# Kernel tuning notes

Hardware: AMD Instinct MI355X
Metric: run time of the kernel (lower is better)

The kernel has to match this reference:

```python
import jax, jax.numpy as jnp
import numpy as np
from jax import lax

B, N, CIN, H, W = 1, 6, 256, 32, 88
COUT = 80
IMG_H, IMG_W = 256, 704
XB = (-51.2, 51.2, 0.8); YB = (-51.2, 51.2, 0.8); ZB = (-5.0, 3.0, 0.8)
NX, NY, NZ = 128, 128, 10
EPS = 1e-5


def _voxel_coords(b0, b1, vs):
    n = int(round((b1 - b0) / vs))
    return jnp.linspace(b0 + 0.5 * vs, b1 - 0.5 * vs, n, dtype=jnp.float32)


def _make_points():
    xs = _voxel_coords(*XB); ys = _voxel_coords(*YB); zs = _voxel_coords(*ZB)
    gx, gy, gz = jnp.meshgrid(xs, ys, zs, indexing='ij')
    return jnp.stack([gx, gy, gz], -1).reshape(-1, 3)  # [M,3], M = NX*NY*NZ


def _conv(x, w, b=None, pad=1):
    y = lax.conv_general_dilated(x, w, (1, 1), [(pad, pad), (pad, pad)],
                                 dimension_numbers=('NCHW', 'OIHW', 'NCHW'))
    if b is not None:
        y = y + b[None, :, None, None]
    return y


def _bn(x, g, b, m, v):
    return (g[None, :, None, None] * (x - m[None, :, None, None])
            * lax.rsqrt(v[None, :, None, None] + EPS) + b[None, :, None, None])


def _bilinear(feat, gx, gy):
    # feat [C,Hf,Wf]; gx,gy [M] in [-1,1]; align_corners=True, zero padding
    C, Hf, Wf = feat.shape
    ix = (gx + 1.0) * 0.5 * (Wf - 1)
    iy = (gy + 1.0) * 0.5 * (Hf - 1)
    ix0 = jnp.floor(ix); iy0 = jnp.floor(iy)
    wx1 = ix - ix0; wy1 = iy - iy0

    def tap(iyf, ixf, wgt):
        valid = (ixf >= 0) & (ixf < Wf) & (iyf >= 0) & (iyf < Hf)
        ii = jnp.clip(ixf, 0, Wf - 1).astype(jnp.int32)
        jj = jnp.clip(iyf, 0, Hf - 1).astype(jnp.int32)
        return feat[:, jj, ii] * (wgt * valid)[None, :]

    return (tap(iy0, ix0, (1 - wy1) * (1 - wx1))
            + tap(iy0, ix0 + 1, (1 - wy1) * wx1)
            + tap(iy0 + 1, ix0, wy1 * (1 - wx1))
            + tap(iy0 + 1, ix0 + 1, wy1 * wx1))


def reference(img, lidar2image, w1, b1, g1, beta1, m1, v1,
              w2, b2, g2, beta2, m2, v2, w3, b3):
    # proj_net: conv3x3+BN+ReLU, conv3x3+BN+ReLU, conv1x1
    x = img.reshape(B * N, CIN, H, W)
    x = jax.nn.relu(_bn(_conv(x, w1, b1), g1, beta1, m1, v1))
    x = jax.nn.relu(_bn(_conv(x, w2, b2), g2, beta2, m2, v2))
    feat = _conv(x, w3, b3, pad=0)  # [B*N, COUT, H, W]

    pts = _make_points()  # [M,3]
    R = lidar2image[:, :, :3, :3].reshape(B * N, 3, 3)
    t = lidar2image[:, :, :3, 3].reshape(B * N, 3, 1)
    proj = jnp.einsum('kij,mj->kim', R, pts) + t  # [BN,3,M]
    dist = proj[:, 2]
    px = proj[:, 0] / dist
    py = proj[:, 1] / dist
    gx = px / IMG_W * 2.0 - 1.0
    gy = py / IMG_H * 2.0 - 1.0

    sampled = jax.vmap(_bilinear)(feat, gx, gy)  # [BN, COUT, M]
    on_img = (px < IMG_W) & (px > 0) & (py < IMG_H) & (py > 0) & (dist > 0.1)
    sampled = jnp.where(on_img[:, None, :], sampled, 0.0)

    vox = sampled.reshape(B, N, COUT, NX, NY, NZ)
    bev = jnp.max(vox, axis=1).mean(axis=-1)  # [B, COUT, NX, NY]
    return bev


def setup_inputs() -> dict:
    key = jax.random.key(0)
    ks = jax.random.split(key, 8)
    img = jax.random.normal(ks[0], (B, N, CIN, H, W), jnp.float32)

    # Plausible lidar->image matrices: 6 cameras in a ring, pinhole intrinsics.
    fx = fy = 280.0; cx = IMG_W / 2.0; cy = IMG_H / 2.0
    K = np.array([[fx, 0.0, cx], [0.0, fy, cy], [0.0, 0.0, 1.0]])
    mats = []
    for k in range(N):
        th = 2.0 * np.pi * k / N
        fwd = np.array([np.cos(th), np.sin(th), 0.0])
        rgt = np.array([np.sin(th), -np.cos(th), 0.0])
        dwn = np.array([0.0, 0.0, -1.0])
        Rm = np.stack([rgt, dwn, fwd], 0)
        c = np.array([0.5 * np.cos(th), 0.5 * np.sin(th), 1.5])
        M4 = np.eye(4)
        M4[:3, :3] = K @ Rm
        M4[:3, 3] = K @ (-Rm @ c)
        mats.append(M4)
    lidar2image = jnp.asarray(np.broadcast_to(np.stack(mats), (B, N, 4, 4)).copy(),
                              jnp.float32)

    def w(k, shape, s=0.02):
        return jax.random.normal(k, shape, jnp.float32) * s

    zc = lambda c: jnp.zeros((c,), jnp.float32)
    oc = lambda c: jnp.ones((c,), jnp.float32)
    return dict(
        img=img, lidar2image=lidar2image,
        w1=w(ks[1], (CIN, CIN, 3, 3)), b1=zc(CIN),
        g1=oc(CIN), beta1=zc(CIN), m1=zc(CIN), v1=oc(CIN),
        w2=w(ks[2], (CIN, CIN, 3, 3)), b2=zc(CIN),
        g2=oc(CIN), beta2=zc(CIN), m2=zc(CIN), v2=oc(CIN),
        w3=w(ks[3], (COUT, CIN, 1, 1)), b3=zc(COUT),
    )
```

## Files before the change

### kernel.cpp

```cpp
#include <hip/hip_runtime.h>
#include <math.h>

#define N_IMG 6
#define CIN   256
#define H_IN  32
#define W_IN  88
#define SP    2816
#define HH    34
#define WW    90
#define SPH   3060
#define COUTC 80
#define EPSBN 1e-5f

typedef _Float16 half8 __attribute__((ext_vector_type(8)));
typedef float floatx4 __attribute__((ext_vector_type(4)));

#define AS1 __attribute__((address_space(1)))
#define AS3 __attribute__((address_space(3)))

__global__ __launch_bounds__(256) void prep_w33(const float* __restrict__ wa,
                                                const float* __restrict__ wb,
                                                _Float16* __restrict__ wTa,
                                                _Float16* __restrict__ wTb) {
  __shared__ float s[2304];
  const int oc = blockIdx.x;
  const int tid = threadIdx.x;
  const float* w = blockIdx.y ? wb : wa;
  _Float16* wT = blockIdx.y ? wTb : wTa;
  const float* wo = w + (size_t)oc * 2304;
  for (int i = tid; i < 2304; i += 256) s[i] = wo[i];
  __syncthreads();
  for (int i = tid; i < 2304; i += 256) {
    const int tap = i >> 8;
    const int ic  = i & 255;
    wT[((size_t)tap * 256 + oc) * 256 + ic] = (_Float16)s[ic * 9 + tap];
  }
}

__global__ __launch_bounds__(256) void prep_misc(const float* __restrict__ w3,
                                                 _Float16* __restrict__ wT3,
                                                 _Float16* __restrict__ a,
                                                 _Float16* __restrict__ b) {
  const int bx = blockIdx.x;
  const int tid = threadIdx.x;
  if (bx < 80) {
    const int idx = bx * 256 + tid;
    wT3[idx] = (_Float16)w3[idx];
  } else {
    const int im = bx - 80;
    for (int s = tid; s < 244 * 32; s += 256) {
      const int pos = s >> 5;
      const int gr  = s & 31;
      int h, w;
      if (pos < 90)       { h = 0;  w = pos; }
      else if (pos < 180) { h = 33; w = pos - 90; }
      else { const int r = pos - 180; h = 1 + (r >> 1); w = (r & 1) * 89; }
      const size_t off = ((size_t)im * SPH + h * WW + w) * CIN + gr * 8;
      half8 z = {};
      *(half8*)(a + off) = z;
      *(half8*)(b + off) = z;
    }
  }
}

__global__ __launch_bounds__(256) void nchw_to_nhwc(const float* __restrict__ img,
                                                    _Float16* __restrict__ x0) {
  __shared__ float t[64][65];
  const int sp0 = blockIdx.x * 64;
  const int ic0 = blockIdx.y * 64;
  const int im  = blockIdx.z;
  const int tx = threadIdx.x & 63;
  const int ty = threadIdx.x >> 6;
  for (int r = ty; r < 64; r += 4)
    t[r][tx] = img[((size_t)(im * CIN + ic0 + r)) * SP + sp0 + tx];
  __syncthreads();
  for (int r = ty; r < 64; r += 4) {
    const int sp = sp0 + r;
    const int h = sp / 88;
    const int w = sp - h * 88;
    x0[((size_t)im * SPH + h * WW + w + WW + 1) * CIN + ic0 + tx] = (_Float16)t[tx][r];
  }
}

__global__ __launch_bounds__(256) void conv3x3_mfma(
    const _Float16* __restrict__ x, const _Float16* __restrict__ wT,
    const float* __restrict__ bias, const float* __restrict__ gamma,
    const float* __restrict__ beta, const float* __restrict__ bnm,
    const float* __restrict__ bnv, _Float16* __restrict__ out,
    int OW, int OB, int imStride)
{
  __shared__ _Float16 As[2][64 * 64];
  __shared__ _Float16 Bs[2][128 * 64];

  const int tid  = threadIdx.x;
  const int wv   = tid >> 6;
  const int lane = tid & 63;
  const int bx   = blockIdx.x;
  const int n0   = (bx & 1) << 7;
  const int mt   = bx >> 1;
  const int im   = mt / 44;
  const int m0sp = (mt - im * 44) * 64;
  const _Float16* xim = x + (size_t)im * SPH * CIN;

  int srcA[2], srcB[4];
  #pragma unroll
  for (int i = 0; i < 2; ++i) {
    const int g = i * 256 + wv * 64 + lane;
    const int row = g >> 3;
    const int lg  = (g & 7) ^ (row & 7);
    const int m = m0sp + row;
    const int h = m / 88;
    const int w = m - h * 88;
    srcA[i] = ((h + 1) * WW + (w + 1)) * CIN + lg * 8;
  }
  #pragma unroll
  for (int i = 0; i < 4; ++i) {
    const int g = i * 256 + wv * 64 + lane;
    const int row = g >> 3;
    const int lg  = (g & 7) ^ (row & 7);
    srcB[i] = (n0 + row) * 256 + lg * 8;
  }

  const int fr = lane & 15;
  const int q  = lane >> 4;
  const int q4 = q * 4;
  const int mw = (wv & 1) * 32;
  const int nw = (wv >> 1) * 64;

  floatx4 acc[2][4];
  #pragma unroll
  for (int i = 0; i < 2; ++i)
    #pragma unroll
    for (int j = 0; j < 4; ++j) {
      acc[i][j][0] = 0.f; acc[i][j][1] = 0.f; acc[i][j][2] = 0.f; acc[i][j][3] = 0.f;
    }

  {
    const int aoff0 = (-1 * WW - 1) * CIN;
    #pragma unroll
    for (int i = 0; i < 2; ++i)
      __builtin_amdgcn_global_load_lds(
          (const AS1 void*)(xim + srcA[i] + aoff0),
          (AS3 void*)(&As[0][(i * 256 + wv * 64) * 8]), 16, 0, 0);
    #pragma unroll
    for (int i = 0; i < 4; ++i)
      __builtin_amdgcn_global_load_lds(
          (const AS1 void*)(wT + srcB[i]),
          (AS3 void*)(&Bs[0][(i * 256 + wv * 64) * 8]), 16, 0, 0);
  }

  for (int c = 0; c < 36; ++c) {
    __syncthreads();
    if (c < 35) {
      const int cn   = c + 1;
      const int tapn = cn >> 2;
      const int iccn = (cn & 3) << 6;
      const int dyn  = tapn / 3 - 1;
      const int dxn  = tapn - (tapn / 3) * 3 - 1;
      const int aoffn = (dyn * WW + dxn) * CIN + iccn;
      const size_t boffn = (size_t)tapn * 65536 + iccn;
      const int nb = cn & 1;
      #pragma unroll
      for (int i = 0; i < 2; ++i)
        __builtin_amdgcn_global_load_lds(
            (const AS1 void*)(xim + srcA[i] + aoffn),
            (AS3 void*)(&As[nb][(i * 256 + wv * 64) * 8]), 16, 0, 0);
      #pragma unroll
      for (int i = 0; i < 4; ++i)
        __builtin_amdgcn_global_load_lds(
            (const AS1 void*)(wT + boffn + srcB[i]),
            (AS3 void*)(&Bs[nb][(i * 256 + wv * 64) * 8]), 16, 0, 0);
    }
    const int cb = c & 1;
    #pragma unroll
    for (int ks = 0; ks < 2; ++ks) {
      half8 af[2], bf[4];
      #pragma unroll
      for (int i = 0; i < 2; ++i) {
        const int row = mw + i * 16 + fr;
        af[i] = *(const half8*)(&As[cb][row * 64 + (((ks * 4 + q) ^ (row & 7)) * 8)]);
      }
      #pragma unroll
      for (int j = 0; j < 4; ++j) {
        const int row = nw + j * 16 + fr;
        bf[j] = *(const half8*)(&Bs[cb][row * 64 + (((ks * 4 + q) ^ (row & 7)) * 8)]);
      }
      #pragma unroll
      for (int i = 0; i < 2; ++i)
        #pragma unroll
        for (int j = 0; j < 4; ++j)
          acc[i][j] = __builtin_amdgcn_mfma_f32_16x16x32_f16(af[i], bf[j], acc[i][j], 0, 0, 0);
    }
  }

  #pragma unroll
  for (int j = 0; j < 4; ++j) {
    const int oc = n0 + nw + j * 16 + fr;
    const float sc = gamma[oc] * rsqrtf(bnv[oc] + EPSBN);
    const float sh = (bias[oc] - bnm[oc]) * sc + beta[oc];
    #pragma unroll
    for (int i = 0; i < 2; ++i) {
      #pragma unroll
      for (int r = 0; r < 4; ++r) {
        const int m = m0sp + mw + i * 16 + q4 + r;
        const int h = m / 88;
        const int w = m - h * 88;
        const float v = fmaxf(fmaf(acc[i][j][r], sc, sh), 0.f);
        out[((size_t)im * imStride + h * OW + w + OB) * CIN + oc] = (_Float16)v;
      }
    }
  }
}

__global__ __launch_bounds__(128) void conv1x1_mfma(
    const _Float16* __restrict__ x, const _Float16* __restrict__ wT,
    const float* __restrict__ bias, _Float16* __restrict__ feat)
{
  __shared__ _Float16 Bs[80 * 264];

  const int tid = threadIdx.x;
  const int m0  = blockIdx.x * 64;
  const int wv   = tid >> 6;
  const int lane = tid & 63;
  const int fr  = lane & 15;
  const int q8  = (lane >> 4) * 8;
  const int q4  = (lane >> 4) * 4;

  for (int g = tid; g < 2560; g += 128) {
    const int oc = g >> 5;
    const int kg8 = (g & 31) << 3;
    *(half8*)(&Bs[oc * 264 + kg8]) = *(const half8*)(wT + oc * 256 + kg8);
  }
  __syncthreads();

  floatx4 acc[2][5];
  #pragma unroll
  for (int i = 0; i < 2; ++i)
    #pragma unroll
    for (int j = 0; j < 5; ++j) {
      acc[i][j][0] = 0.f; acc[i][j][1] = 0.f; acc[i][j][2] = 0.f; acc[i][j][3] = 0.f;
    }

  const _Float16* xa = x + (size_t)(m0 + wv * 32 + fr) * 256 + q8;
  #pragma unroll
  for (int ks = 0; ks < 8; ++ks) {
    half8 af[2], bf[5];
    #pragma unroll
    for (int i = 0; i < 2; ++i)
      af[i] = *(const half8*)(xa + (size_t)i * 16 * 256 + ks * 32);
    #pragma unroll
    for (int j = 0; j < 5; ++j)
      bf[j] = *(const half8*)(&Bs[(j * 16 + fr) * 264 + ks * 32 + q8]);
    #pragma unroll
    for (int i = 0; i < 2; ++i)
      #pragma unroll
      for (int j = 0; j < 5; ++j)
        acc[i][j] = __builtin_amdgcn_mfma_f32_16x16x32_f16(af[i], bf[j], acc[i][j], 0, 0, 0);
  }

  #pragma unroll
  for (int j = 0; j < 5; ++j) {
    const int oc = j * 16 + fr;
    const float bb = bias[oc];
    #pragma unroll
    for (int i = 0; i < 2; ++i) {
      const int mbase = m0 + wv * 32 + i * 16 + q4;
      #pragma unroll
      for (int r = 0; r < 4; ++r)
        feat[(size_t)(mbase + r) * COUTC + oc] = (_Float16)(acc[i][j][r] + bb);
    }
  }
}

__global__ __launch_bounds__(320) void bev_sample(
    const _Float16* __restrict__ feat, const float* __restrict__ l2i,
    float* __restrict__ tmp)
{
  __shared__ int4   eo[1920];
  __shared__ float4 ew[1920];
  const int tid = threadIdx.x;
  const int cellBase = blockIdx.x * 32;

  for (int e = tid; e < 1920; e += 320) {
    const int cell = e / 60;
    const int idx = e - cell * 60;
    const int n = idx / 10;
    const int z = idx - n * 10;
    const int cid = cellBase + cell;
    const int gix = cid >> 7;
    const int giy = cid & 127;
    const float X = (float)(-50.8 + (double)gix * (101.6 / 127.0));
    const float Y = (float)(-50.8 + (double)giy * (101.6 / 127.0));
    const float Z = (float)(-4.6 + (double)z * (7.2 / 9.0));
    const float* M = l2i + n * 16;
    const float pw = M[0] * X + M[1] * Y + M[2] * Z + M[3];
    const float ph = M[4] * X + M[5] * Y + M[6] * Z + M[7];
    const float d  = M[8] * X + M[9] * Y + M[10] * Z + M[11];
    const float px = pw / d;
    const float py = ph / d;
    const bool on_img = (px < 704.f) && (px > 0.f) && (py < 256.f) && (py > 0.f) && (d > 0.1f);
    const float gx = px / 704.f * 2.f - 1.f;
    const float gy = py / 256.f * 2.f - 1.f;
    const float ixf = (gx + 1.f) * 0.5f * 87.f;
    const float iyf = (gy + 1.f) * 0.5f * 31.f;
    const float ix0 = floorf(ixf);
    const float iy0 = floorf(iyf);
    const float wx1 = ixf - ix0;
    const float wy1 = iyf - iy0;
    const float ix1 = ix0 + 1.f, iy1 = iy0 + 1.f;
    float w00 = (1.f - wy1) * (1.f - wx1);
    float w01 = (1.f - wy1) * wx1;
    float w10 = wy1 * (1.f - wx1);
    float w11 = wy1 * wx1;
    const bool vx0 = (ix0 >= 0.f) && (ix0 < 88.f);
    const bool vx1 = (ix1 >= 0.f) && (ix1 < 88.f);
    const bool vy0 = (iy0 >= 0.f) && (iy0 < 32.f);
    const bool vy1 = (iy1 >= 0.f) && (iy1 < 32.f);
    if (!(on_img && vy0 && vx0)) w00 = 0.f;
    if (!(on_img && vy0 && vx1)) w01 = 0.f;
    if (!(on_img && vy1 && vx0)) w10 = 0.f;
    if (!(on_img && vy1 && vx1)) w11 = 0.f;
    const int i0 = (int)fminf(fmaxf(ix0, 0.f), 87.f);
    const int i1 = (int)fminf(fmaxf(ix1, 0.f), 87.f);
    const int j0 = (int)fminf(fmaxf(iy0, 0.f), 31.f);
    const int j1 = (int)fminf(fmaxf(iy1, 0.f), 31.f);
    const int base = n * SP;
    eo[e] = make_int4((base + j0 * 88 + i0) * COUTC,
                      (base + j0 * 88 + i1) * COUTC,
                      (base + j1 * 88 + i0) * COUTC,
                      (base + j1 * 88 + i1) * COUTC);
    ew[e] = make_float4(w00, w01, w10, w11);
  }
  __syncthreads();

  const int grp  = tid % 10;
  const int c8   = grp * 8;
  const int cell = tid / 10;
  const int ebase = cell * 60;
  float acc[8];
  #pragma unroll
  for (int k = 0; k < 8; ++k) acc[k] = 0.f;

  for (int z = 0; z < 10; ++z) {
    float mx[8];
    #pragma unroll
    for (int k = 0; k < 8; ++k) mx[k] = -INFINITY;
    #pragma unroll
    for (int n = 0; n < 6; ++n) {
      const float4 w = ew[ebase + n * 10 + z];
      if (w.x + w.y + w.z + w.w > 0.f) {
        const int4 o = eo[ebase + n * 10 + z];
        const half8 p00 = *(const half8*)(feat + o.x + c8);
        const half8 p01 = *(const half8*)(feat + o.y + c8);
        const half8 p10 = *(const half8*)(feat + o.z + c8);
        const half8 p11 = *(const half8*)(feat + o.w + c8);
        #pragma unroll
        for (int k = 0; k < 8; ++k) {
          float v = w.x * (float)p00[k];
          v = fmaf(w.y, (float)p01[k], v);
          v = fmaf(w.z, (float)p10[k], v);
          v = fmaf(w.w, (float)p11[k], v);
          mx[k] = fmaxf(mx[k], v);
        }
      } else {
        #pragma unroll
        for (int k = 0; k < 8; ++k) mx[k] = fmaxf(mx[k], 0.f);
      }
    }
    #pragma unroll
    for (int k = 0; k < 8; ++k) acc[k] += mx[k];
  }
  const int cid = cellBase + cell;
  float* op = tmp + (size_t)cid * COUTC + c8;
  #pragma unroll
  for (int k = 0; k < 8; ++k) op[k] = acc[k] * 0.1f;
}

__global__ __launch_bounds__(256) void bev_transpose(const float* __restrict__ tmp,
                                                     float* __restrict__ out)
{
  __shared__ float tile[32][33];
  const int mBase = blockIdx.x * 32;
  const int cBase = blockIdx.y * 32;
  const int tx = threadIdx.x & 31;
  const int ty = threadIdx.x >> 5;
  for (int i = ty; i < 32; i += 8) {
    const int cc = cBase + tx;
    tile[i][tx] = (cc < COUTC) ? tmp[(size_t)(mBase + i) * COUTC + cc] : 0.f;
  }
  __syncthreads();
  for (int i = ty; i < 32; i += 8) {
    const int cc = cBase + i;
    if (cc < COUTC) out[(size_t)cc * 16384 + mBase + tx] = tile[tx][i];
  }
}

extern "C" void kernel_launch(void* const* d_in, const int* in_sizes, int n_in,
                              void* d_out, int out_size, void* d_ws, size_t ws_size,
                              hipStream_t stream)
{
  const float* img = (const float*)d_in[0];
  const float* l2i = (const float*)d_in[1];
  const float* w1  = (const float*)d_in[2];
  const float* b1  = (const float*)d_in[3];
  const float* g1  = (const float*)d_in[4];
  const float* be1 = (const float*)d_in[5];
  const float* m1  = (const float*)d_in[6];
  const float* v1  = (const float*)d_in[7];
  const float* w2  = (const float*)d_in[8];
  const float* b2  = (const float*)d_in[9];
  const float* g2  = (const float*)d_in[10];
  const float* be2 = (const float*)d_in[11];
  const float* m2  = (const float*)d_in[12];
  const float* v2  = (const float*)d_in[13];
  const float* w3  = (const float*)d_in[14];
  const float* b3  = (const float*)d_in[15];

  char* ws = (char*)d_ws;
  _Float16* wT1h = (_Float16*)ws;  ws += (size_t)9 * CIN * CIN * 2;
  _Float16* wT2h = (_Float16*)ws;  ws += (size_t)9 * CIN * CIN * 2;
  _Float16* wT3h = (_Float16*)ws;  ws += (size_t)CIN * COUTC * 2;
  _Float16* x0   = (_Float16*)ws;  ws += (size_t)N_IMG * SPH * CIN * 2;
  _Float16* x1h  = (_Float16*)ws;  ws += (size_t)N_IMG * SPH * CIN * 2;
  _Float16* x2h  = (_Float16*)ws;  ws += (size_t)N_IMG * SP * CIN * 2;
  _Float16* feat = (_Float16*)ws;  ws += (size_t)N_IMG * SP * COUTC * 2;
  float*    tmp  = (float*)ws;
  float*    outp = (float*)d_out;

  prep_misc<<<86, 256, 0, stream>>>(w3, wT3h, x0, x1h);
  prep_w33<<<dim3(256, 2), 256, 0, stream>>>(w1, w2, wT1h, wT2h);
  nchw_to_nhwc<<<dim3(44, 4, 6), 256, 0, stream>>>(img, x0);

  conv3x3_mfma<<<528, 256, 0, stream>>>(x0, wT1h, b1, g1, be1, m1, v1,
                                        x1h, WW, WW + 1, SPH);
  conv3x3_mfma<<<528, 256, 0, stream>>>(x1h, wT2h, b2, g2, be2, m2, v2,
                                        x2h, 88, 0, SP);
  conv1x1_mfma<<<264, 128, 0, stream>>>(x2h, wT3h, b3, feat);

  bev_sample<<<512, 320, 0, stream>>>(feat, l2i, tmp);
  bev_transpose<<<dim3(512, 3), 256, 0, stream>>>(tmp, outp);
}
```

Measured before the change: 221.9 us.

## Split conv3x3 reduction over K into three partials with separate BN reduce

Each 3x3 conv's 36-step K loop is split across three blocks (blockIdx.y), raising the grid from 528 to 1584 blocks so more of the 256 CUs stay busy. Each split writes fp16 partial sums to a workspace buffer, and a new reduce_bn kernel adds the three partials, applies bias, BN and ReLU, and writes the padded NHWC output. The cost is extra global traffic for the partials (about 26 MB written and read per conv), two extra launches, and some precision loss from rounding partials to fp16.

```diff
diff --git a/kernel.cpp b/kernel.cpp
--- a/kernel.cpp
+++ b/kernel.cpp
@@ -82,12 +82,9 @@
   }
 }
 
-__global__ __launch_bounds__(256) void conv3x3_mfma(
+__global__ __launch_bounds__(256) void conv3x3_split(
     const _Float16* __restrict__ x, const _Float16* __restrict__ wT,
-    const float* __restrict__ bias, const float* __restrict__ gamma,
-    const float* __restrict__ beta, const float* __restrict__ bnm,
-    const float* __restrict__ bnv, _Float16* __restrict__ out,
-    int OW, int OB, int imStride)
+    _Float16* __restrict__ part)
 {
   __shared__ _Float16 As[2][64 * 64];
   __shared__ _Float16 Bs[2][128 * 64];
@@ -96,6 +93,7 @@
   const int wv   = tid >> 6;
   const int lane = tid & 63;
   const int bx   = blockIdx.x;
+  const int s    = blockIdx.y;
   const int n0   = (bx & 1) << 7;
   const int mt   = bx >> 1;
   const int im   = mt / 44;
@@ -135,8 +133,15 @@
       acc[i][j][0] = 0.f; acc[i][j][1] = 0.f; acc[i][j][2] = 0.f; acc[i][j][3] = 0.f;
     }
 
+  const int c0 = s * 12;
+
   {
-    const int aoff0 = (-1 * WW - 1) * CIN;
+    const int tap0 = c0 >> 2;
+    const int icc0 = (c0 & 3) << 6;
+    const int dy0  = tap0 / 3 - 1;
+    const int dx0  = tap0 - (tap0 / 3) * 3 - 1;
+    const int aoff0 = (dy0 * WW + dx0) * CIN + icc0;
+    const size_t boff0 = (size_t)tap0 * 65536 + icc0;
     #pragma unroll
     for (int i = 0; i < 2; ++i)
       __builtin_amdgcn_global_load_lds(
@@ -145,21 +150,21 @@
     #pragma unroll
     for (int i = 0; i < 4; ++i)
       __builtin_amdgcn_global_load_lds(
-          (const AS1 void*)(wT + srcB[i]),
+          (const AS1 void*)(wT + boff0 + srcB[i]),
           (AS3 void*)(&Bs[0][(i * 256 + wv * 64) * 8]), 16, 0, 0);
   }
 
-  for (int c = 0; c < 36; ++c) {
+  for (int lc = 0; lc < 12; ++lc) {
     __syncthreads();
-    if (c < 35) {
-      const int cn   = c + 1;
+    if (lc < 11) {
+      const int cn   = c0 + lc + 1;
       const int tapn = cn >> 2;
       const int iccn = (cn & 3) << 6;
       const int dyn  = tapn / 3 - 1;
       const int dxn  = tapn - (tapn / 3) * 3 - 1;
       const int aoffn = (dyn * WW + dxn) * CIN + iccn;
       const size_t boffn = (size_t)tapn * 65536 + iccn;
-      const int nb = cn & 1;
+      const int nb = (lc + 1) & 1;
       #pragma unroll
       for (int i = 0; i < 2; ++i)
         __builtin_amdgcn_global_load_lds(
@@ -171,7 +176,7 @@
             (const AS1 void*)(wT + boffn + srcB[i]),
             (AS3 void*)(&Bs[nb][(i * 256 + wv * 64) * 8]), 16, 0, 0);
     }
-    const int cb = c & 1;
+    const int cb = lc & 1;
     #pragma unroll
     for (int ks = 0; ks < 2; ++ks) {
       half8 af[2], bf[4];
@@ -193,23 +198,57 @@
     }
   }
 
+  _Float16* pb = part + ((size_t)s * 16896 + im * 2816 + m0sp) * 256;
   #pragma unroll
   for (int j = 0; j < 4; ++j) {
     const int oc = n0 + nw + j * 16 + fr;
-    const float sc = gamma[oc] * rsqrtf(bnv[oc] + EPSBN);
-    const float sh = (bias[oc] - bnm[oc]) * sc + beta[oc];
     #pragma unroll
     for (int i = 0; i < 2; ++i) {
       #pragma unroll
       for (int r = 0; r < 4; ++r) {
-        const int m = m0sp + mw + i * 16 + q4 + r;
-        const int h = m / 88;
-        const int w = m - h * 88;
-        const float v = fmaxf(fmaf(acc[i][j][r], sc, sh), 0.f);
-        out[((size_t)im * imStride + h * OW + w + OB) * CIN + oc] = (_Float16)v;
+        const int mloc = mw + i * 16 + q4 + r;
+        pb[(size_t)mloc * 256 + oc] = (_Float16)acc[i][j][r];
       }
     }
   }
+}
+
+__global__ __launch_bounds__(256) void reduce_bn(
+    const _Float16* __restrict__ part, const float* __restrict__ bias,
+    const float* __restrict__ gamma, const float* __restrict__ beta,
+    const float* __restrict__ bnm, const float* __restrict__ bnv,
+    _Float16* __restrict__ out, int OW, int OB, int imStride)
+{
+  __shared__ float scs[256], shs[256];
+  const int tid = threadIdx.x;
+  {
+    const float sc = gamma[tid] * rsqrtf(bnv[tid] + EPSBN);
+    scs[tid] = sc;
+    shs[tid] = (bias[tid] - bnm[tid]) * sc + beta[tid];
+  }
+  __syncthreads();
+
+  const int e   = blockIdx.x * 256 + tid;
+  const int oc8 = (e & 31) * 8;
+  const int m   = e >> 5;
+  const int im  = m / 2816;
+  const int sp  = m - im * 2816;
+  const int h   = sp / 88;
+  const int w   = sp - h * 88;
+
+  const size_t base = (size_t)m * 256 + oc8;
+  const half8 p0 = *(const half8*)(part + base);
+  const half8 p1 = *(const half8*)(part + base + (size_t)16896 * 256);
+  const half8 p2 = *(const half8*)(part + base + (size_t)2 * 16896 * 256);
+
+  half8 o;
+  #pragma unroll
+  for (int k = 0; k < 8; ++k) {
+    const int oc = oc8 + k;
+    const float v = (float)p0[k] + (float)p1[k] + (float)p2[k];
+    o[k] = (_Float16)fmaxf(fmaf(v, scs[oc], shs[oc]), 0.f);
+  }
+  *(half8*)(out + ((size_t)im * imStride + h * OW + w + OB) * CIN + oc8) = o;
 }
 
 __global__ __launch_bounds__(128) void conv1x1_mfma(
@@ -423,6 +462,7 @@
   _Float16* x0   = (_Float16*)ws;  ws += (size_t)N_IMG * SPH * CIN * 2;
   _Float16* x1h  = (_Float16*)ws;  ws += (size_t)N_IMG * SPH * CIN * 2;
   _Float16* x2h  = (_Float16*)ws;  ws += (size_t)N_IMG * SP * CIN * 2;
+  _Float16* part = (_Float16*)ws;  ws += (size_t)3 * 16896 * 256 * 2;
   _Float16* feat = (_Float16*)ws;  ws += (size_t)N_IMG * SP * COUTC * 2;
   float*    tmp  = (float*)ws;
   float*    outp = (float*)d_out;
@@ -431,10 +471,12 @@
   prep_w33<<<dim3(256, 2), 256, 0, stream>>>(w1, w2, wT1h, wT2h);
   nchw_to_nhwc<<<dim3(44, 4, 6), 256, 0, stream>>>(img, x0);
 
-  conv3x3_mfma<<<528, 256, 0, stream>>>(x0, wT1h, b1, g1, be1, m1, v1,
-                                        x1h, WW, WW + 1, SPH);
-  conv3x3_mfma<<<528, 256, 0, stream>>>(x1h, wT2h, b2, g2, be2, m2, v2,
-                                        x2h, 88, 0, SP);
+  conv3x3_split<<<dim3(528, 3), 256, 0, stream>>>(x0, wT1h, part);
+  reduce_bn<<<2112, 256, 0, stream>>>(part, b1, g1, be1, m1, v1,
+                                      x1h, WW, WW + 1, SPH);
+  conv3x3_split<<<dim3(528, 3), 256, 0, stream>>>(x1h, wT2h, part);
+  reduce_bn<<<2112, 256, 0, stream>>>(part, b2, g2, be2, m2, v2,
+                                      x2h, 88, 0, SP);
   conv1x1_mfma<<<264, 128, 0, stream>>>(x2h, wT3h, b3, feat);
 
   bev_sample<<<512, 320, 0, stream>>>(feat, l2i, tmp);
```

New measurement: 242.2 us. 1.09x slower.

## Load conv weights directly into registers and double K-chunk per LDS stage

Applied to the files above, without the earlier changes.

The 3x3 conv kernel no longer stages the weight (B) tile through shared memory. Each lane now reads its MFMA B fragments straight from global memory, with the first fragment of the next chunk prefetched into registers. The activation tile in LDS grows to 128 channels per stage, which halves the number of barrier-separated iterations from 36 to 18, and the swizzle is adapted to the wider rows. The aim is lower LDS traffic and fewer syncs. The cost is global-load latency on the MFMA critical path for the weights, which relies on L1/L2 caching because every M-tile block re-reads the same weights.

```diff
diff --git a/kernel.cpp b/kernel.cpp
--- a/kernel.cpp
+++ b/kernel.cpp
@@ -89,8 +89,7 @@
     const float* __restrict__ bnv, _Float16* __restrict__ out,
     int OW, int OB, int imStride)
 {
-  __shared__ _Float16 As[2][64 * 64];
-  __shared__ _Float16 Bs[2][128 * 64];
+  __shared__ _Float16 As[2][64 * 128];
 
   const int tid  = threadIdx.x;
   const int wv   = tid >> 6;
@@ -102,31 +101,31 @@
   const int m0sp = (mt - im * 44) * 64;
   const _Float16* xim = x + (size_t)im * SPH * CIN;
 
-  int srcA[2], srcB[4];
-  #pragma unroll
-  for (int i = 0; i < 2; ++i) {
+  int srcA[4];
+  #pragma unroll
+  for (int i = 0; i < 4; ++i) {
     const int g = i * 256 + wv * 64 + lane;
-    const int row = g >> 3;
-    const int lg  = (g & 7) ^ (row & 7);
-    const int m = m0sp + row;
+    const int r = g >> 4;
+    const int p = g & 15;
+    const int l = (p & 8) | ((p ^ r) & 7);
+    const int m = m0sp + r;
     const int h = m / 88;
     const int w = m - h * 88;
-    srcA[i] = ((h + 1) * WW + (w + 1)) * CIN + lg * 8;
-  }
-  #pragma unroll
-  for (int i = 0; i < 4; ++i) {
-    const int g = i * 256 + wv * 64 + lane;
-    const int row = g >> 3;
-    const int lg  = (g & 7) ^ (row & 7);
-    srcB[i] = (n0 + row) * 256 + lg * 8;
+    srcA[i] = ((h + 1) * WW + (w + 1)) * CIN + l * 8;
   }
 
   const int fr = lane & 15;
   const int q  = lane >> 4;
+  const int q8 = q * 8;
   const int q4 = q * 4;
   const int mw = (wv & 1) * 32;
   const int nw = (wv >> 1) * 64;
 
+  const _Float16* wB[4];
+  #pragma unroll
+  for (int j = 0; j < 4; ++j)
+    wB[j] = wT + (size_t)(n0 + nw + j * 16 + fr) * 256 + q8;
+
   floatx4 acc[2][4];
   #pragma unroll
   for (int i = 0; i < 2; ++i)
@@ -138,58 +137,65 @@
   {
     const int aoff0 = (-1 * WW - 1) * CIN;
     #pragma unroll
-    for (int i = 0; i < 2; ++i)
+    for (int i = 0; i < 4; ++i)
       __builtin_amdgcn_global_load_lds(
           (const AS1 void*)(xim + srcA[i] + aoff0),
           (AS3 void*)(&As[0][(i * 256 + wv * 64) * 8]), 16, 0, 0);
-    #pragma unroll
-    for (int i = 0; i < 4; ++i)
-      __builtin_amdgcn_global_load_lds(
-          (const AS1 void*)(wT + srcB[i]),
-          (AS3 void*)(&Bs[0][(i * 256 + wv * 64) * 8]), 16, 0, 0);
-  }
-
-  for (int c = 0; c < 36; ++c) {
+  }
+  half8 bpre[4];
+  #pragma unroll
+  for (int j = 0; j < 4; ++j) bpre[j] = *(const half8*)(wB[j]);
+
+  for (int c = 0; c < 18; ++c) {
     __syncthreads();
-    if (c < 35) {
+    if (c < 17) {
       const int cn   = c + 1;
-      const int tapn = cn >> 2;
-      const int iccn = (cn & 3) << 6;
+      const int tapn = cn >> 1;
+      const int iccn = (cn & 1) << 7;
       const int dyn  = tapn / 3 - 1;
       const int dxn  = tapn - (tapn / 3) * 3 - 1;
       const int aoffn = (dyn * WW + dxn) * CIN + iccn;
-      const size_t boffn = (size_t)tapn * 65536 + iccn;
       const int nb = cn & 1;
       #pragma unroll
-      for (int i = 0; i < 2; ++i)
+      for (int i = 0; i < 4; ++i)
         __builtin_amdgcn_global_load_lds(
             (const AS1 void*)(xim + srcA[i] + aoffn),
             (AS3 void*)(&As[nb][(i * 256 + wv * 64) * 8]), 16, 0, 0);
-      #pragma unroll
-      for (int i = 0; i < 4; ++i)
-        __builtin_amdgcn_global_load_lds(
-            (const AS1 void*)(wT + boffn + srcB[i]),
-            (AS3 void*)(&Bs[nb][(i * 256 + wv * 64) * 8]), 16, 0, 0);
-    }
-    const int cb = c & 1;
-    #pragma unroll
-    for (int ks = 0; ks < 2; ++ks) {
+    }
+    const int tap = c >> 1;
+    const int icc = (c & 1) << 7;
+    const size_t bco = (size_t)tap * 65536 + icc;
+    const _Float16* Ac = As[c & 1];
+
+    #pragma unroll
+    for (int ks = 0; ks < 4; ++ks) {
       half8 af[2], bf[4];
       #pragma unroll
       for (int i = 0; i < 2; ++i) {
         const int row = mw + i * 16 + fr;
-        af[i] = *(const half8*)(&As[cb][row * 64 + (((ks * 4 + q) ^ (row & 7)) * 8)]);
+        const int l = ks * 4 + q;
+        const int p = (l & 8) | ((l ^ row) & 7);
+        af[i] = *(const half8*)(&Ac[row * 128 + p * 8]);
       }
-      #pragma unroll
-      for (int j = 0; j < 4; ++j) {
-        const int row = nw + j * 16 + fr;
-        bf[j] = *(const half8*)(&Bs[cb][row * 64 + (((ks * 4 + q) ^ (row & 7)) * 8)]);
+      if (ks == 0) {
+        #pragma unroll
+        for (int j = 0; j < 4; ++j) bf[j] = bpre[j];
+      } else {
+        #pragma unroll
+        for (int j = 0; j < 4; ++j) bf[j] = *(const half8*)(wB[j] + bco + ks * 32);
       }
       #pragma unroll
       for (int i = 0; i < 2; ++i)
         #pragma unroll
         for (int j = 0; j < 4; ++j)
           acc[i][j] = __builtin_amdgcn_mfma_f32_16x16x32_f16(af[i], bf[j], acc[i][j], 0, 0, 0);
+    }
+
+    if (c < 17) {
+      const int cn   = c + 1;
+      const size_t bcn = (size_t)(cn >> 1) * 65536 + ((cn & 1) << 7);
+      #pragma unroll
+      for (int j = 0; j < 4; ++j) bpre[j] = *(const half8*)(wB[j] + bcn);
     }
   }
 
```

New measurement: 362.0 us. 1.63x slower.
